# Optimization experiments

Hardware: AMD Instinct MI355X
Metric: run time of the kernel (lower is better)

## Reference

```python
import jax, jax.numpy as jnp
import numpy as np
import functools

N, D, R, E, L, C, MAXDEG = 40000, 128, 3, 640000, 2, 40, 512
BN_EPS = 1e-5


def setup_inputs():
    ks = iter(jax.random.split(jax.random.key(0), 40))
    nrm = lambda s, sc=0.05: jax.random.normal(next(ks), s, dtype=jnp.float32) * sc
    x = jax.random.normal(next(ks), (N, D), dtype=jnp.float32)
    edge_indices = jax.random.randint(next(ks), (R, 2, E), 0, N, dtype=jnp.int32)
    out_emb = nrm((L, MAXDEG, D)).at[:, 0].set(0.0)  # padding_idx=0 -> zero row
    in_emb = nrm((L, MAXDEG, D)).at[:, 0].set(0.0)
    return dict(
        x=x, edge_indices=edge_indices,
        W_src=nrm((L, D, D)), b_src=nrm((L, D)),
        W_dst=nrm((L, D, D)), b_dst=nrm((L, D)),
        W_outf=nrm((L, D)), b_outf=nrm((L,)),
        W_inf=nrm((L, D)), b_inf=nrm((L,)),
        W_fc=nrm((L, D, D)), b_fc=nrm((L, D)),
        bn_gamma=jnp.ones((L, D), jnp.float32), bn_beta=jnp.zeros((L, D), jnp.float32),
        out_deg_emb=out_emb, in_deg_emb=in_emb,
        out_mask=jnp.ones((R, N), jnp.float32), out_mask_bias=jnp.zeros((R, N), jnp.float32),
        in_mask=jnp.ones((R, N), jnp.float32), in_mask_bias=jnp.zeros((R, N), jnp.float32),
        alpha=jnp.float32(0.5), tau=jnp.float32(0.0),
        W_lin=nrm((D, C)), b_lin=nrm((C,)),
    )


def _forward(x, W_src, b_src, W_dst, b_dst, W_outf, b_outf, W_inf, b_inf,
             W_fc, b_fc, bn_gamma, bn_beta, out_deg_emb, in_deg_emb,
             out_mask, out_mask_bias, in_mask, in_mask_bias, alpha, tau,
             W_lin, b_lin, edge_indices):
    seg = lambda d, i: jax.ops.segment_sum(d, i, num_segments=N)
    # source builds I with arange(0, N-1): identity with last diagonal entry missing
    i_mask = (jnp.arange(N) < N - 1).astype(jnp.float32)[:, None]

    rel = []
    for r in range(R):
        row, col = edge_indices[r, 0], edge_indices[r, 1]
        ones = jnp.ones(E, jnp.float32)
        out_deg, in_deg = seg(ones, row), seg(ones, col)
        ods = jnp.where(out_deg > 0, 1.0 / jnp.sqrt(jnp.maximum(out_deg, 1.0)), 0.0)
        ids_ = jnp.where(in_deg > 0, 1.0 / jnp.sqrt(jnp.maximum(in_deg, 1.0)), 0.0)
        # 'dir' norm: D_out^{-1/2} A D_in^{-1/2}; the transposed adj shares the same edge weights
        w = ods[row] * ids_[col]
        rel.append((row, col, w,
                    jnp.clip(out_deg, 0, MAXDEG - 1).astype(jnp.int32),
                    jnp.clip(in_deg, 0, MAXDEG - 1).astype(jnp.int32)))

    def spmm(r_, y):  # adj_norm @ y : gather cols, scatter-add to rows
        row, col, w = rel[r_][0], rel[r_][1], rel[r_][2]
        return seg(w[:, None] * y[col], row)

    def spmm_t(r_, y):  # adj_norm^T @ y
        row, col, w = rel[r_][0], rel[r_][1], rel[r_][2]
        return seg(w[:, None] * y[row], col)

    def dirichlet(mm, y):
        x1 = y / (jnp.sum(jnp.abs(y), axis=1, keepdims=True) + 1e-12)  # row_l1_normalize
        x1sq = x1 * x1
        return (i_mask * x1sq + mm(x1sq)) - 2.0 * ((i_mask * x1 + mm(x1)) * x1 - x1sq)

    eff_tau = jnp.exp(tau) + 0.1

    def conv(l, h):
        out = jnp.zeros((N, D), h.dtype)
        cis, cos_ = [], []
        for r in range(R):
            mm = functools.partial(spmm, r)
            mmt = functools.partial(spmm_t, r)
            out_nei, in_nei = mm(h), mmt(h)
            e_out, e_in = dirichlet(mm, h), dirichlet(mmt, h)
            c_out = (-e_out + out_deg_emb[l][rel[r][3]]) @ W_outf[l] + b_outf[l]  # [N]
            c_in = (-e_in + in_deg_emb[l][rel[r][4]]) @ W_inf[l] + b_inf[l]
            cm = jax.nn.softmax(jnp.stack([c_out, c_in], axis=1) / eff_tau, axis=1)  # tau_softmax
            c_out = cm[:, 0] * out_mask[r] + out_mask_bias[r]
            c_in = cm[:, 1] * in_mask[r] + in_mask_bias[r]
            out = out + c_out[:, None] * (out_nei @ W_src[l] + b_src[l]) \
                      + c_in[:, None] * (in_nei @ W_dst[l] + b_dst[l])
            cis.append(c_in)
            cos_.append(c_out)
        out = out / R
        # F.pad(x,(0,dim-x.shape[1])) is a no-op since input_dim == output_dim
        output = out + alpha * (h @ W_fc[l] + b_fc[l])
        mu, var = jnp.mean(output, axis=0), jnp.var(output, axis=0)  # BatchNorm1d (train mode)
        output = (output - mu) / jnp.sqrt(var + BN_EPS) * bn_gamma[l] + bn_beta[l]
        return output, jnp.mean(jnp.stack(cis), 0)[:, None], jnp.mean(jnp.stack(cos_), 0)[:, None]

    pos_h, neg_h = x, x
    pos_hs, neg_hs, gs, cins, couts = [], [], [], [], []
    for l in range(L):
        ph, ci, co = conv(l, pos_h)
        ph = jax.nn.relu(ph)  # jumping_knowledge truthy -> relu every layer; dropout p=0
        perm = jax.random.permutation(jax.random.key(100 + l), N)  # torch.randperm
        nh, _, _ = conv(l, neg_h[perm])
        nh = jax.nn.relu(nh)
        pos_h, neg_h = ph, nh
        pos_hs.append(ph)
        neg_hs.append(nh)
        gs.append(jnp.mean(ph, axis=0, keepdims=True))
        cins.append(ci)
        couts.append(co)
    c_ins = jnp.mean(jnp.stack(cins), 0)
    c_outs = jnp.mean(jnp.stack(couts), 0)
    jk = functools.reduce(jnp.maximum, pos_hs)  # JumpingKnowledge mode='max'
    logp = jax.nn.log_softmax(jk @ W_lin + b_lin, axis=1)
    return (logp, c_ins, c_outs, *pos_hs, *neg_hs, *gs)


def reference(x, edge_indices, W_src, b_src, W_dst, b_dst, W_outf, b_outf,
              W_inf, b_inf, W_fc, b_fc, bn_gamma, bn_beta, out_deg_emb,
              in_deg_emb, out_mask, out_mask_bias, in_mask, in_mask_bias,
              alpha, tau, W_lin, b_lin):
    return _forward(x, W_src, b_src, W_dst, b_dst, W_outf, b_outf, W_inf, b_inf,
                    W_fc, b_fc, bn_gamma, bn_beta, out_deg_emb, in_deg_emb,
                    out_mask, out_mask_bias, in_mask, in_mask_bias, alpha, tau,
                    W_lin, b_lin, edge_indices)
```

## Files before the change

### kernel.cpp

```cpp
#include <hip/hip_runtime.h>

constexpr int Nn = 40000;
constexpr int Dd = 128;
constexpr int Rr = 3;
constexpr int Ee = 640000;
constexpr int Ll = 2;
constexpr int Cc = 40;
constexpr int MAXD = 512;
constexpr float BN_EPS = 1e-5f;

constexpr int RB_ELEMS = 1024;
constexpr int RB_NB = (Nn + RB_ELEMS - 1) / RB_ELEMS;
constexpr int RB_BINS = 256;
constexpr int RB_H = RB_BINS * RB_NB;

constexpr int EB_ELEMS = 4096;
constexpr int EB_NB = (Ee + EB_ELEMS - 1) / EB_ELEMS;
constexpr int EB_H = 256 * EB_NB;

constexpr int HR_BINS = 13334;
constexpr int HR_PAD = 13344;
constexpr int HR_SB = 16;
constexpr int HR_CHUNK = (Ee + HR_SB - 1) / HR_SB;

__device__ __forceinline__ unsigned rotl32(unsigned x, int d) { return (x << d) | (x >> (32 - d)); }

__device__ void threefry2x32(unsigned k0, unsigned k1, unsigned c0, unsigned c1,
                             unsigned& o0, unsigned& o1) {
  unsigned ks2 = k0 ^ k1 ^ 0x1BD11BDAu;
  unsigned x0 = c0 + k0, x1 = c1 + k1;
#define TFR4(a,b,c,d2) \
  x0 += x1; x1 = rotl32(x1,a);  x1 ^= x0; \
  x0 += x1; x1 = rotl32(x1,b);  x1 ^= x0; \
  x0 += x1; x1 = rotl32(x1,c);  x1 ^= x0; \
  x0 += x1; x1 = rotl32(x1,d2); x1 ^= x0;
  TFR4(13,15,26,6);  x0 += k1;  x1 += ks2 + 1u;
  TFR4(17,29,16,24); x0 += ks2; x1 += k0 + 2u;
  TFR4(13,15,26,6);  x0 += k0;  x1 += k1 + 3u;
  TFR4(17,29,16,24); x0 += k1;  x1 += ks2 + 4u;
  TFR4(13,15,26,6);  x0 += ks2; x1 += k0 + 5u;
#undef TFR4
  o0 = x0; o1 = x1;
}

__global__ void k_genkeys2(unsigned* __restrict__ keys, unsigned seed0, unsigned seed1,
                           int rounds, int* __restrict__ vout, int doIota) {
  int i = blockIdx.x * blockDim.x + threadIdx.x;
  if (i >= 2 * Nn) return;
  int seg = i / Nn, li = i - seg * Nn;
  unsigned seed = seg ? seed1 : seed0;
  unsigned k0 = 0u, k1 = seed, sk0 = 0u, sk1 = 0u;
  for (int rd = 0; rd < rounds; rd++) {
    unsigned a0, a1, b0, b1;
    threefry2x32(k0, k1, 0u, 0u, a0, a1);
    threefry2x32(k0, k1, 0u, 1u, b0, b1);
    sk0 = b0; sk1 = b1;
    k0 = a0; k1 = a1;
  }
  unsigned o0, o1;
  threefry2x32(sk0, sk1, 0u, (unsigned)li, o0, o1);
  keys[i] = o0 ^ o1;
  if (doIota) vout[i] = li;
}

__global__ void k_rhist2(const unsigned* __restrict__ keys, int* __restrict__ hist, int shift) {
  __shared__ int lh[RB_BINS];
  int a = blockIdx.x / RB_NB, blk = blockIdx.x % RB_NB;
  const unsigned* src = keys + (size_t)a * Nn;
  int t = threadIdx.x;
  lh[t] = 0;
  __syncthreads();
  int base = blk * RB_ELEMS;
  for (int i = t; i < RB_ELEMS; i += 256) {
    int g = base + i;
    if (g < Nn) atomicAdd(&lh[(src[g] >> shift) & 255], 1);
  }
  __syncthreads();
  hist[(size_t)a * RB_H + t * RB_NB + blk] = lh[t];
}

__device__ void scan_body(const int* cnt, int* off, int n, int items) {
  int t = threadIdx.x;
  int lo = t * items, hi = min(lo + items, n);
  int s = 0;
  for (int i = lo; i < hi; i++) s += cnt[i];
  int lane = t & 63, wid = t >> 6;
  int sc = s;
#pragma unroll
  for (int o = 1; o < 64; o <<= 1) {
    int v = __shfl_up(sc, o);
    if (lane >= o) sc += v;
  }
  __shared__ int wsum[16], woff[16];
  if (lane == 63) wsum[wid] = sc;
  __syncthreads();
  if (t == 0) {
    int a = 0;
    for (int w = 0; w < 16; w++) { woff[w] = a; a += wsum[w]; }
    off[n] = a;
  }
  __syncthreads();
  int run = woff[wid] + sc - s;
  for (int i = lo; i < hi; i++) {
    int v = cnt[i];
    off[i] = run;
    run += v;
  }
}

__global__ __launch_bounds__(1024) void k_scanP(const int* __restrict__ hist, int* __restrict__ esc) {
  int a = blockIdx.x;
  scan_body(hist + (size_t)a * RB_H, esc + (size_t)a * (RB_H + 1), RB_H, (RB_H + 1023) / 1024);
}

__global__ __launch_bounds__(1024) void k_scan6(const int* __restrict__ odeg, const int* __restrict__ ideg,
                                                int* __restrict__ csr_off, int* __restrict__ csc_off) {
  int b = blockIdx.x;
  const int* cnt = (b < 3) ? (odeg + b * Nn) : (ideg + (b - 3) * Nn);
  int* off = (b < 3) ? (csr_off + b * (Nn + 1)) : (csc_off + (b - 3) * (Nn + 1));
  scan_body(cnt, off, Nn, (Nn + 1023) / 1024);
}

__global__ void k_rscatter2(const unsigned* __restrict__ keys, const int* __restrict__ vals,
                            const int* __restrict__ scanned, int shift,
                            unsigned* __restrict__ okeys, int* __restrict__ ovals) {
  __shared__ int running[RB_BINS];
  __shared__ int wcount[4][RB_BINS];
  __shared__ int dbase[RB_BINS];
  int a = blockIdx.x / RB_NB, blk = blockIdx.x % RB_NB;
  const unsigned* ksrc = keys + (size_t)a * Nn;
  const int* vsrc = vals + (size_t)a * Nn;
  unsigned* kdst = okeys + (size_t)a * Nn;
  int* vdst = ovals + (size_t)a * Nn;
  int t = threadIdx.x;
  int lane = t & 63, w = t >> 6;
  running[t] = 0;
  dbase[t] = scanned[(size_t)a * (RB_H + 1) + t * RB_NB + blk];
  int base = blk * RB_ELEMS;
  for (int rnd = 0; rnd < 4; rnd++) {
#pragma unroll
    for (int q = 0; q < 4; q++) wcount[q][t] = 0;
    __syncthreads();
    int g = base + rnd * 256 + t;
    bool valid = g < Nn;
    unsigned key = valid ? ksrc[g] : 0u;
    int d = (key >> shift) & 255;
    unsigned long long bb = __ballot(valid);
    unsigned long long mask = bb;
#pragma unroll
    for (int k = 0; k < 8; k++) {
      bool b = (d >> k) & 1;
      unsigned long long tt = __ballot(b && valid);
      mask &= b ? tt : ~tt;
    }
    mask &= bb;
    int riw = __popcll(mask & ((1ull << lane) - 1ull));
    int cnt_ = __popcll(mask);
    if (valid && riw == 0) wcount[w][d] = cnt_;
    __syncthreads();
    if (valid) {
      int prior = 0;
#pragma unroll
      for (int ww = 0; ww < 4; ww++) if (ww < w) prior += wcount[ww][d];
      int gp = dbase[d] + running[d] + prior + riw;
      kdst[gp] = key;
      vdst[gp] = vsrc[g];
    }
    __syncthreads();
    running[t] += wcount[0][t] + wcount[1][t] + wcount[2][t] + wcount[3][t];
    __syncthreads();
  }
}

__global__ void k_permrows(const float* __restrict__ src, const int* __restrict__ perm,
                           float* __restrict__ dst) {
  int row = blockIdx.x * 8 + (threadIdx.x >> 5);
  int lane = threadIdx.x & 31;
  if (row >= Nn) return;
  int p = perm[row];
  ((float4*)(dst + (size_t)row * Dd))[lane] = ((const float4*)(src + (size_t)p * Dd))[lane];
}

__global__ __launch_bounds__(256) void k_hist2(const int* __restrict__ ei, int* __restrict__ partials) {
  __shared__ int lh[HR_BINS];
  int bid = blockIdx.x;
  int sb = bid % HR_SB;
  int range = (bid / HR_SB) % 3;
  int j = bid / (3 * HR_SB);
  int rel = j >> 1, which = j & 1;
  const int* src = ei + (size_t)rel * 2 * Ee + (size_t)which * Ee;
  int lo = range * HR_BINS;
  for (int i = threadIdx.x; i < HR_BINS; i += 256) lh[i] = 0;
  __syncthreads();
  int e0 = sb * HR_CHUNK, e1 = min(e0 + HR_CHUNK, Ee);
  for (int e = e0 + threadIdx.x; e < e1; e += 256) {
    int v = src[e] - lo;
    if (v >= 0 && v < HR_BINS) atomicAdd(&lh[v], 1);
  }
  __syncthreads();
  int* dst = partials + (size_t)bid * HR_PAD;
  for (int i = threadIdx.x; i < HR_BINS; i += 256) dst[i] = lh[i];
}

__global__ void k_hreduce(const int* __restrict__ partials, int* __restrict__ odeg,
                          int* __restrict__ ideg) {
  int idx = blockIdx.x * 256 + threadIdx.x;
  if (idx >= 6 * Nn) return;
  int j = idx / Nn, bin = idx - j * Nn;
  int range = bin / HR_BINS, off = bin - range * HR_BINS;
  const int* p = partials + (size_t)((j * 3 + range) * HR_SB) * HR_PAD + off;
  int sum = 0;
#pragma unroll
  for (int b = 0; b < HR_SB; b++) sum += p[(size_t)b * HR_PAD];
  int rel = j >> 1;
  (j & 1 ? ideg : odeg)[rel * Nn + bin] = sum;
}

__global__ void k_degnorm(const int* __restrict__ odeg, const int* __restrict__ ideg,
                          float* __restrict__ ods, float* __restrict__ ids,
                          int* __restrict__ odix, int* __restrict__ idix) {
  int idx = blockIdx.x * blockDim.x + threadIdx.x;
  if (idx >= Rr * Nn) return;
  int od = odeg[idx], id_ = ideg[idx];
  ods[idx] = od > 0 ? 1.0f / sqrtf((float)od) : 0.0f;
  ids[idx] = id_ > 0 ? 1.0f / sqrtf((float)id_) : 0.0f;
  odix[idx] = od < MAXD - 1 ? od : MAXD - 1;
  idix[idx] = id_ < MAXD - 1 ? id_ : MAXD - 1;
}

__global__ void k_pack(const int* __restrict__ ei, unsigned* __restrict__ pcsr,
                       unsigned* __restrict__ pcsc) {
  int idx = blockIdx.x * 256 + threadIdx.x;
  if (idx >= 3 * Ee) return;
  int r = idx / Ee, e = idx - r * Ee;
  const int* base = ei + (size_t)r * 2 * Ee;
  unsigned rw = (unsigned)base[e], cl = (unsigned)base[Ee + e];
  pcsr[idx] = (rw << 16) | cl;
  pcsc[idx] = (cl << 16) | rw;
}

__global__ __launch_bounds__(256) void k_ehist(const unsigned* __restrict__ pin,
                                               int* __restrict__ hist, int shift) {
  __shared__ int lh[256];
  int a = blockIdx.x / EB_NB, blk = blockIdx.x % EB_NB;
  const unsigned* src = pin + (size_t)a * Ee;
  lh[threadIdx.x] = 0;
  __syncthreads();
  int base = blk * EB_ELEMS;
  for (int i = threadIdx.x; i < EB_ELEMS; i += 256) {
    int g = base + i;
    if (g < Ee) atomicAdd(&lh[(src[g] >> shift) & 255], 1);
  }
  __syncthreads();
  hist[(size_t)a * EB_H + threadIdx.x * EB_NB + blk] = lh[threadIdx.x];
}

__global__ __launch_bounds__(1024) void k_escan6(const int* __restrict__ hist, int* __restrict__ esc) {
  int a = blockIdx.x;
  scan_body(hist + (size_t)a * EB_H, esc + (size_t)a * (EB_H + 1), EB_H, (EB_H + 1023) / 1024);
}

__global__ __launch_bounds__(256) void k_escatter(const unsigned* __restrict__ pin,
                                                  const int* __restrict__ esc, int shift,
                                                  unsigned* __restrict__ pout) {
  __shared__ int running[256];
  __shared__ int wcount[4][256];
  __shared__ int dbase[256];
  int a = blockIdx.x / EB_NB, blk = blockIdx.x % EB_NB;
  const unsigned* src = pin + (size_t)a * Ee;
  unsigned* dst = pout + (size_t)a * Ee;
  int t = threadIdx.x;
  int lane = t & 63, w = t >> 6;
  running[t] = 0;
  dbase[t] = esc[(size_t)a * (EB_H + 1) + t * EB_NB + blk];
  int base = blk * EB_ELEMS;
  for (int rnd = 0; rnd < 16; rnd++) {
#pragma unroll
    for (int q = 0; q < 4; q++) wcount[q][t] = 0;
    __syncthreads();
    int g = base + rnd * 256 + t;
    bool valid = g < Ee;
    unsigned key = valid ? src[g] : 0u;
    int d = (key >> shift) & 255;
    unsigned long long bb = __ballot(valid);
    unsigned long long mask = bb;
#pragma unroll
    for (int k = 0; k < 8; k++) {
      bool b = (d >> k) & 1;
      unsigned long long tt = __ballot(b && valid);
      mask &= b ? tt : ~tt;
    }
    mask &= bb;
    int riw = __popcll(mask & ((1ull << lane) - 1ull));
    int cnt_ = __popcll(mask);
    if (valid && riw == 0) wcount[w][d] = cnt_;
    __syncthreads();
    if (valid) {
      int prior = 0;
#pragma unroll
      for (int ww = 0; ww < 4; ww++) if (ww < w) prior += wcount[ww][d];
      int gp = dbase[d] + running[d] + prior + riw;
      dst[gp] = key;
    }
    __syncthreads();
    running[t] += wcount[0][t] + wcount[1][t] + wcount[2][t] + wcount[3][t];
    __syncthreads();
  }
}

__global__ void k_rowscalar(const float* __restrict__ h, const float* __restrict__ Wfo,
                            const float* __restrict__ Wfi, float4* __restrict__ aux,
                            const float* __restrict__ ods, const float* __restrict__ ids,
                            float4* __restrict__ auxrd,
                            float* __restrict__ bnsum, float* __restrict__ gs) {
  if (blockIdx.x == 0) {
    bnsum[threadIdx.x] = 0.f;
    if (gs != nullptr && threadIdx.x < Dd) gs[threadIdx.x] = 0.f;
  }
  int wid = (blockIdx.x * blockDim.x + threadIdx.x) >> 6;
  int lane = threadIdx.x & 63;
  if (wid >= Nn) return;
  float2 a = ((const float2*)(h + (size_t)wid * Dd))[lane];
  float2 wo = ((const float2*)Wfo)[lane];
  float2 wi = ((const float2*)Wfi)[lane];
  float l1 = fabsf(a.x) + fabsf(a.y);
  float so = a.x * a.x * wo.x + a.y * a.y * wo.y;
  float si = a.x * a.x * wi.x + a.y * a.y * wi.y;
#pragma unroll
  for (int o = 32; o; o >>= 1) {
    l1 += __shfl_xor(l1, o);
    so += __shfl_xor(so, o);
    si += __shfl_xor(si, o);
  }
  if (lane == 0) {
    float ri = 1.0f / (l1 + 1e-12f);
    float qo = ri * ri * so, qi = ri * ri * si;
    aux[wid] = make_float4(ri, qo, qi, 0.f);
#pragma unroll
    for (int r = 0; r < Rr; r++) {
      auxrd[(size_t)(2 * r) * Nn + wid] = make_float4(ids[r * Nn + wid], ri, qo, 0.f);
      auxrd[(size_t)(2 * r + 1) * Nn + wid] = make_float4(ods[r * Nn + wid], ri, qi, 0.f);
    }
  }
}

__global__ void k_lut2(const float* __restrict__ eo, const float* __restrict__ ei_,
                       const float* __restrict__ W_outf, const float* __restrict__ W_inf,
                       float* __restrict__ luto, float* __restrict__ luti) {
  int wid = (blockIdx.x * blockDim.x + threadIdx.x) >> 6;
  int lane = threadIdx.x & 63;
  if (wid >= 2 * MAXD) return;
  int l = wid >> 9, k = wid & (MAXD - 1);
  float2 a = ((const float2*)(eo + ((size_t)l * MAXD + k) * Dd))[lane];
  float2 b = ((const float2*)(ei_ + ((size_t)l * MAXD + k) * Dd))[lane];
  float2 wo = ((const float2*)(W_outf + l * Dd))[lane];
  float2 wi = ((const float2*)(W_inf + l * Dd))[lane];
  float so = a.x * wo.x + a.y * wo.y;
  float si = b.x * wi.x + b.y * wi.y;
#pragma unroll
  for (int o = 32; o; o >>= 1) { so += __shfl_xor(so, o); si += __shfl_xor(si, o); }
  if (lane == 0) { luto[wid] = so; luti[wid] = si; }
}

__global__ __launch_bounds__(256) void k_csrdir3(
    const int* __restrict__ csr_off, const unsigned* __restrict__ pcsr,
    const int* __restrict__ csc_off, const unsigned* __restrict__ pcsc,
    const float* __restrict__ ods_r, const float* __restrict__ ids_r,
    const float4* __restrict__ auxo, const float4* __restrict__ auxi,
    const float4* __restrict__ aux, const float* __restrict__ h,
    const float* __restrict__ Wfo, const float* __restrict__ Wfi,
    const float* __restrict__ luto, const float* __restrict__ luti,
    const int* __restrict__ odix, const int* __restrict__ idix,
    const float* __restrict__ bo, const float* __restrict__ bi,
    const float* __restrict__ taup,
    const float* __restrict__ omask, const float* __restrict__ omaskb,
    const float* __restrict__ imask, const float* __restrict__ imaskb,
    float* __restrict__ Tout, float* __restrict__ Tin,
    float* __restrict__ sco, float* __restrict__ sci,
    float* __restrict__ co_acc, float* __restrict__ ci_acc,
    int first, int is_pos) {
  __shared__ float lq[4], lp[4], lc[4];
  int t = threadIdx.x;
  int wv = t >> 6, lane = t & 63;
  int dir = wv >> 1;
  int n = blockIdx.x * 2 + (wv & 1);
  const int* off = dir ? csc_off : csr_off;
  const unsigned* nbrp = dir ? pcsc : pcsr;
  const float4* auxd = dir ? auxi : auxo;
  float a_self = (dir ? ids_r : ods_r)[n];
  const float* Wf = dir ? Wfi : Wfo;
  int s0 = off[n], s1 = off[n + 1];
  int hl = lane & 31, half = lane >> 5;
  float4 wf4 = ((const float4*)Wf)[hl];
  float4 hn4 = ((const float4*)(h + (size_t)n * Dd))[hl];
  float rn = aux[n].x;
  float4 s = make_float4(0.f, 0.f, 0.f, 0.f);
  float4 pa = make_float4(0.f, 0.f, 0.f, 0.f);
  float qacc = 0.f;
  for (int base = s0; base < s1; base += 64) {
    int eidx = base + lane;
    bool valid = eidx < s1;
    int mi = valid ? (int)(nbrp[eidx] & 0xFFFFu) : 0;
    float4 av = valid ? auxd[mi] : make_float4(0.f, 0.f, 0.f, 0.f);
    int cnt = min(64, s1 - base);
#pragma unroll 4
    for (int j = half; j < cnt; j += 2) {
      int m = __shfl(mi, j);
      float sc = __shfl(av.x, j);
      float rm = __shfl(av.y, j);
      float qv = __shfl(av.z, j);
      float w = a_self * sc;
      float wrm = w * rm;
      float4 hv = ((const float4*)(h + (size_t)m * Dd))[hl];
      s.x += w * hv.x; s.y += w * hv.y; s.z += w * hv.z; s.w += w * hv.w;
      pa.x += wrm * hv.x; pa.y += wrm * hv.y; pa.z += wrm * hv.z; pa.w += wrm * hv.w;
      qacc += w * qv;
    }
  }
  s.x += __shfl_xor(s.x, 32); s.y += __shfl_xor(s.y, 32);
  s.z += __shfl_xor(s.z, 32); s.w += __shfl_xor(s.w, 32);
  pa.x += __shfl_xor(pa.x, 32); pa.y += __shfl_xor(pa.y, 32);
  pa.z += __shfl_xor(pa.z, 32); pa.w += __shfl_xor(pa.w, 32);
  qacc += __shfl_xor(qacc, 32);
  float pd = rn * (hn4.x * wf4.x * pa.x + hn4.y * wf4.y * pa.y +
                   hn4.z * wf4.z * pa.z + hn4.w * wf4.w * pa.w);
#pragma unroll
  for (int o = 16; o; o >>= 1) pd += __shfl_xor(pd, o);
  if (lane == 0) { lq[wv] = qacc; lp[wv] = pd; }
  __syncthreads();
  if (t < 2) {
    int nn = blockIdx.x * 2 + t;
    float Qo_ = lq[t], Po_ = lp[t], Qi_ = lq[2 + t], Pi_ = lp[2 + t];
    float4 a2 = aux[nn];
    float im = (nn < Nn - 1) ? 1.0f : 0.0f;
    float so_ = luto[odix[nn]] + bo[0] - (Qo_ - 2.0f * Po_ + (2.0f - im) * a2.y);
    float si_ = luti[idix[nn]] + bi[0] - (Qi_ - 2.0f * Pi_ + (2.0f - im) * a2.z);
    float tt = expf(taup[0]) + 0.1f;
    float aa = so_ / tt, bb = si_ / tt;
    float mm = fmaxf(aa, bb);
    float ea = expf(aa - mm), eb = expf(bb - mm);
    float inv = 1.0f / (ea + eb);
    float co = ea * inv * omask[nn] + omaskb[nn];
    float ci = eb * inv * imask[nn] + imaskb[nn];
    lc[t] = co; lc[2 + t] = ci;
    if (first) { sco[nn] = co; sci[nn] = ci; }
    else       { sco[nn] += co; sci[nn] += ci; }
    if (is_pos) { co_acc[nn] += co; ci_acc[nn] += ci; }
  }
  __syncthreads();
  float c = lc[wv];
  if (lane < 32) {
    float* T = dir ? Tin : Tout;
    size_t o = (size_t)n * Dd;
    float4 v = make_float4(c * s.x, c * s.y, c * s.z, c * s.w);
    if (!first) {
      float4 old = ((const float4*)(T + o))[hl];
      v.x += old.x; v.y += old.y; v.z += old.z; v.w += old.w;
    }
    ((float4*)(T + o))[hl] = v;
  }
}

__global__ __launch_bounds__(256) void k_gemmconv(
    const float* __restrict__ Tout, const float* __restrict__ Tin, const float* __restrict__ h,
    const float* __restrict__ Wsrc, const float* __restrict__ Wdst, const float* __restrict__ Wfc,
    const float* __restrict__ bsrc, const float* __restrict__ bdst, const float* __restrict__ bfc,
    const float* __restrict__ sco, const float* __restrict__ sci,
    const float* __restrict__ alphap, float* __restrict__ pre, float* __restrict__ bnsum) {
  __shared__ float Asm[64][36];
  __shared__ float Bsm[32][132];
  __shared__ float lsum[128], lsum2[128];
  int t = threadIdx.x;
  int rg = t >> 5, cg = t & 31;
  int m0 = blockIdx.x * 64;
  int arow = t >> 2, aq = t & 3;
  float alpha = alphap[0];
  float acc[8][4];
#pragma unroll
  for (int r = 0; r < 8; r++)
#pragma unroll
    for (int c = 0; c < 4; c++) acc[r][c] = 0.f;
  for (int kt = 0; kt < 12; kt++) {
    int sec = kt >> 2, kc = (kt & 3) * 32;
    const float* Ap = sec == 0 ? Tout : (sec == 1 ? Tin : h);
    const float* Wp = sec == 0 ? Wsrc : (sec == 1 ? Wdst : Wfc);
    float sA = (sec == 2) ? alpha : (1.0f / (float)Rr);
    __syncthreads();
    {
      const float4* src = (const float4*)(Ap + (size_t)(m0 + arow) * Dd + kc + aq * 8);
      float4 v0 = src[0], v1 = src[1];
      float4* d0 = (float4*)&Asm[arow][aq * 8];
      d0[0] = make_float4(v0.x * sA, v0.y * sA, v0.z * sA, v0.w * sA);
      d0[1] = make_float4(v1.x * sA, v1.y * sA, v1.z * sA, v1.w * sA);
    }
#pragma unroll
    for (int j = 0; j < 4; j++) {
      int idx = t + j * 256;
      int k = idx >> 5, d4 = idx & 31;
      *(float4*)&Bsm[k][d4 * 4] = *(const float4*)(Wp + (size_t)(kc + k) * Dd + d4 * 4);
    }
    __syncthreads();
#pragma unroll
    for (int kk = 0; kk < 32; kk += 4) {
      float4 af[8], bf[4];
#pragma unroll
      for (int r = 0; r < 8; r++) af[r] = *(const float4*)&Asm[rg * 8 + r][kk];
#pragma unroll
      for (int j = 0; j < 4; j++) bf[j] = *(const float4*)&Bsm[kk + j][cg * 4];
#pragma unroll
      for (int r = 0; r < 8; r++) {
        const float* ap = (const float*)&af[r];
#pragma unroll
        for (int j = 0; j < 4; j++) {
          const float* bp = (const float*)&bf[j];
          acc[r][0] += ap[j] * bp[0];
          acc[r][1] += ap[j] * bp[1];
          acc[r][2] += ap[j] * bp[2];
          acc[r][3] += ap[j] * bp[3];
        }
      }
    }
  }
  float4 vb1 = *(const float4*)(bsrc + cg * 4);
  float4 vb2 = *(const float4*)(bdst + cg * 4);
  float4 vbf = *(const float4*)(bfc + cg * 4);
  float ps[4] = {0.f, 0.f, 0.f, 0.f}, ps2[4] = {0.f, 0.f, 0.f, 0.f};
#pragma unroll
  for (int r = 0; r < 8; r++) {
    int row = m0 + rg * 8 + r;
    size_t o = (size_t)row * Dd + cg * 4;
    float s1 = sco[row] * (1.0f / (float)Rr), s2 = sci[row] * (1.0f / (float)Rr);
    float4 v;
    v.x = acc[r][0] + s1 * vb1.x + s2 * vb2.x + alpha * vbf.x;
    v.y = acc[r][1] + s1 * vb1.y + s2 * vb2.y + alpha * vbf.y;
    v.z = acc[r][2] + s1 * vb1.z + s2 * vb2.z + alpha * vbf.z;
    v.w = acc[r][3] + s1 * vb1.w + s2 * vb2.w + alpha * vbf.w;
    *(float4*)(pre + o) = v;
    ps[0] += v.x; ps[1] += v.y; ps[2] += v.z; ps[3] += v.w;
    ps2[0] += v.x * v.x; ps2[1] += v.y * v.y; ps2[2] += v.z * v.z; ps2[3] += v.w * v.w;
  }
  if (t < 128) { lsum[t] = 0.f; lsum2[t] = 0.f; }
  __syncthreads();
#pragma unroll
  for (int j = 0; j < 4; j++) {
    atomicAdd(&lsum[cg * 4 + j], ps[j]);
    atomicAdd(&lsum2[cg * 4 + j], ps2[j]);
  }
  __syncthreads();
  if (t < 128) atomicAdd(&bnsum[t], lsum[t]);
  else if (t < 256) atomicAdd(&bnsum[t], lsum2[t - 128]);
}

__global__ void k_bnapply(const float* __restrict__ pre, const float* __restrict__ sums,
                          const float* __restrict__ gamma, const float* __restrict__ beta,
                          float* __restrict__ hout, float* __restrict__ gs, int do_gs) {
  __shared__ float ls[256];
  int c = threadIdx.x & 127, sub = threadIdx.x >> 7;
  float mu = sums[c] * (1.0f / (float)Nn);
  float var = sums[c + 128] * (1.0f / (float)Nn) - mu * mu;
  float sc = gamma[c] / sqrtf(var + BN_EPS);
  float bt = beta[c];
  float g = 0.f;
  for (int n = blockIdx.x * 2 + sub; n < Nn; n += gridDim.x * 2) {
    float v = (pre[(size_t)n * Dd + c] - mu) * sc + bt;
    v = fmaxf(v, 0.f);
    hout[(size_t)n * Dd + c] = v;
    g += v;
  }
  if (do_gs) {
    ls[threadIdx.x] = g;
    __syncthreads();
    if (sub == 0) atomicAdd(&gs[c], (ls[c] + ls[c + 128]) * (1.0f / (float)Nn));
  }
}

__global__ __launch_bounds__(64) void k_logp(const float* __restrict__ ph0, const float* __restrict__ ph1,
                      const float* __restrict__ Wlin, const float* __restrict__ blin,
                      const float* __restrict__ ci_acc, const float* __restrict__ co_acc,
                      float* __restrict__ cins, float* __restrict__ couts,
                      float* __restrict__ logp) {
  __shared__ float jk[Dd];
  __shared__ float lg[Cc];
  int n = blockIdx.x, t = threadIdx.x;
  if (t == 63) {
    cins[n] = ci_acc[n] * (1.0f / (float)(Ll * Rr));
    couts[n] = co_acc[n] * (1.0f / (float)(Ll * Rr));
  }
  for (int d = t; d < Dd; d += 64) jk[d] = fmaxf(ph0[(size_t)n * Dd + d], ph1[(size_t)n * Dd + d]);
  __syncthreads();
  if (t < Cc) {
    float acc = blin[t];
    for (int k = 0; k < Dd; k++) acc += jk[k] * Wlin[k * Cc + t];
    lg[t] = acc;
  }
  __syncthreads();
  float m = -1e30f;
  for (int c = 0; c < Cc; c++) m = fmaxf(m, lg[c]);
  float s = 0.f;
  for (int c = 0; c < Cc; c++) s += expf(lg[c] - m);
  float lse = m + logf(s);
  if (t < Cc) logp[(size_t)n * Cc + t] = lg[t] - lse;
}

extern "C" void kernel_launch(void* const* d_in, const int* in_sizes, int n_in,
                              void* d_out, int out_size, void* d_ws, size_t ws_size,
                              hipStream_t stream) {
  const float* x      = (const float*)d_in[0];
  const int*   ei     = (const int*)d_in[1];
  const float* W_src  = (const float*)d_in[2];
  const float* b_src  = (const float*)d_in[3];
  const float* W_dst  = (const float*)d_in[4];
  const float* b_dst  = (const float*)d_in[5];
  const float* W_outf = (const float*)d_in[6];
  const float* b_outf = (const float*)d_in[7];
  const float* W_inf  = (const float*)d_in[8];
  const float* b_inf  = (const float*)d_in[9];
  const float* W_fc   = (const float*)d_in[10];
  const float* b_fc   = (const float*)d_in[11];
  const float* gamma  = (const float*)d_in[12];
  const float* beta   = (const float*)d_in[13];
  const float* oemb   = (const float*)d_in[14];
  const float* iemb   = (const float*)d_in[15];
  const float* omask  = (const float*)d_in[16];
  const float* omaskb = (const float*)d_in[17];
  const float* imask  = (const float*)d_in[18];
  const float* imaskb = (const float*)d_in[19];
  const float* alphap = (const float*)d_in[20];
  const float* taup   = (const float*)d_in[21];
  const float* Wlin   = (const float*)d_in[22];
  const float* blin   = (const float*)d_in[23];

  float* out   = (float*)d_out;
  float* logp  = out;
  float* cins  = logp + (size_t)Nn * Cc;
  float* couts = cins + Nn;
  float* ph0   = couts + Nn;
  float* ph1   = ph0 + (size_t)Nn * Dd;
  float* nh0   = ph1 + (size_t)Nn * Dd;
  float* nh1   = nh0 + (size_t)Nn * Dd;
  float* gs0   = nh1 + (size_t)Nn * Dd;
  float* gs1   = gs0 + Dd;

  char* p = (char*)d_ws;
  auto alloc = [&](size_t bytes) -> void* {
    void* q = (void*)p;
    p += (bytes + 255) & ~(size_t)255;
    return q;
  };
  float* pre   = (float*)alloc((size_t)Nn * Dd * 4);
  float* Tout  = (float*)alloc((size_t)Nn * Dd * 4);
  float* Tin   = (float*)alloc((size_t)Nn * Dd * 4);
  float* hperm = (float*)alloc((size_t)Nn * Dd * 4);
  unsigned* pbuf = (unsigned*)alloc((size_t)6 * Ee * 4);
  size_t qwords = (size_t)6 * Ee;
  size_t pwords = (size_t)(6 * 3 * HR_SB) * HR_PAD;
  unsigned* qbuf = (unsigned*)alloc((qwords > pwords ? qwords : pwords) * 4);
  int* partials = (int*)qbuf;
  int* csr_off = (int*)alloc((size_t)Rr * (Nn + 1) * 4);
  int* csc_off = (int*)alloc((size_t)Rr * (Nn + 1) * 4);
  int* odeg    = (int*)alloc((size_t)Rr * Nn * 4);
  int* ideg    = (int*)alloc((size_t)Rr * Nn * 4);
  float* ods   = (float*)alloc((size_t)Rr * Nn * 4);
  float* ids   = (float*)alloc((size_t)Rr * Nn * 4);
  int* odix    = (int*)alloc((size_t)Rr * Nn * 4);
  int* idix    = (int*)alloc((size_t)Rr * Nn * 4);
  float4* aux  = (float4*)alloc((size_t)Nn * 16);
  float4* auxrd = (float4*)alloc((size_t)6 * Nn * 16);
  float* sco   = (float*)alloc((size_t)Nn * 4 * 2);
  float* sci   = sco + Nn;
  float* coacc = (float*)alloc((size_t)Nn * 4 * 2);
  float* ciacc = coacc + Nn;
  float* luto  = (float*)alloc((size_t)2 * MAXD * 4);
  float* luti  = (float*)alloc((size_t)2 * MAXD * 4);
  float* bnsum = (float*)alloc(256 * 4);
  unsigned* kbuf0 = (unsigned*)alloc((size_t)2 * Nn * 4);
  unsigned* kbuf1 = (unsigned*)alloc((size_t)2 * Nn * 4);
  int* vbuf0 = (int*)alloc((size_t)2 * Nn * 4);
  int* vbuf1 = (int*)alloc((size_t)2 * Nn * 4);
  int* rhist = (int*)alloc((size_t)2 * (RB_H + 1) * 4);
  int* rscan = (int*)alloc((size_t)2 * (RB_H + 1) * 4);
  int* ehist = (int*)alloc((size_t)6 * EB_H * 4);
  int* escan = (int*)alloc((size_t)6 * (EB_H + 1) * 4);

  k_hist2<<<6 * 3 * HR_SB, 256, 0, stream>>>(ei, partials);
  k_hreduce<<<(6 * Nn + 255) / 256, 256, 0, stream>>>(partials, odeg, ideg);
  k_degnorm<<<(Rr * Nn + 255) / 256, 256, 0, stream>>>(odeg, ideg, ods, ids, odix, idix);
  k_scan6<<<6, 1024, 0, stream>>>(odeg, ideg, csr_off, csc_off);
  k_pack<<<(3 * Ee + 255) / 256, 256, 0, stream>>>(ei, pbuf, pbuf + (size_t)3 * Ee);
  k_ehist<<<6 * EB_NB, 256, 0, stream>>>(pbuf, ehist, 16);
  k_escan6<<<6, 1024, 0, stream>>>(ehist, escan);
  k_escatter<<<6 * EB_NB, 256, 0, stream>>>(pbuf, escan, 16, qbuf);
  k_ehist<<<6 * EB_NB, 256, 0, stream>>>(qbuf, ehist, 24);
  k_escan6<<<6, 1024, 0, stream>>>(ehist, escan);
  k_escatter<<<6 * EB_NB, 256, 0, stream>>>(qbuf, escan, 24, pbuf);
  hipMemsetAsync(coacc, 0, (size_t)Nn * 4 * 2, stream);
  k_lut2<<<2 * MAXD / 4, 256, 0, stream>>>(oemb, iemb, W_outf, W_inf, luto, luti);

  auto radix4b = [&]() {
    for (int pass = 0; pass < 4; pass++) {
      const unsigned* ik = (pass & 1) ? kbuf1 : kbuf0;
      const int*      iv = (pass & 1) ? vbuf1 : vbuf0;
      unsigned*       ok = (pass & 1) ? kbuf0 : kbuf1;
      int*            ov = (pass & 1) ? vbuf0 : vbuf1;
      int shift = pass * 8;
      k_rhist2<<<2 * RB_NB, 256, 0, stream>>>(ik, rhist, shift);
      k_scanP<<<2, 1024, 0, stream>>>(rhist, rscan);
      k_rscatter2<<<2 * RB_NB, 256, 0, stream>>>(ik, iv, rscan, shift, ok, ov);
    }
  };
  k_genkeys2<<<(2 * Nn + 255) / 256, 256, 0, stream>>>(kbuf0, 100u, 101u, 1, vbuf0, 1);
  radix4b();
  k_genkeys2<<<(2 * Nn + 255) / 256, 256, 0, stream>>>(kbuf0, 100u, 101u, 2, vbuf0, 0);
  radix4b();

  auto conv = [&](int l, const float* hin, float* hout, float* gs, int is_pos) {
    const float* Wfo = W_outf + l * Dd;
    const float* Wfi = W_inf + l * Dd;
    k_rowscalar<<<Nn / 4, 256, 0, stream>>>(hin, Wfo, Wfi, aux, ods, ids, auxrd, bnsum,
                                            is_pos ? gs : nullptr);
    for (int r = 0; r < Rr; r++) {
      k_csrdir3<<<Nn / 2, 256, 0, stream>>>(csr_off + r * (Nn + 1), pbuf + (size_t)r * Ee,
                                            csc_off + r * (Nn + 1), pbuf + (size_t)(3 + r) * Ee,
                                            ods + r * Nn, ids + r * Nn,
                                            auxrd + (size_t)(2 * r) * Nn,
                                            auxrd + (size_t)(2 * r + 1) * Nn,
                                            aux, hin, Wfo, Wfi,
                                            luto + l * MAXD, luti + l * MAXD,
                                            odix + r * Nn, idix + r * Nn,
                                            b_outf + l, b_inf + l, taup,
                                            omask + (size_t)r * Nn, omaskb + (size_t)r * Nn,
                                            imask + (size_t)r * Nn, imaskb + (size_t)r * Nn,
                                            Tout, Tin, sco, sci, coacc, ciacc,
                                            r == 0 ? 1 : 0, is_pos);
    }
    k_gemmconv<<<Nn / 64, 256, 0, stream>>>(Tout, Tin, hin,
                                            W_src + (size_t)l * Dd * Dd, W_dst + (size_t)l * Dd * Dd,
                                            W_fc + (size_t)l * Dd * Dd,
                                            b_src + l * Dd, b_dst + l * Dd, b_fc + l * Dd,
                                            sco, sci, alphap, pre, bnsum);
    k_bnapply<<<256, 256, 0, stream>>>(pre, bnsum, gamma + l * Dd, beta + l * Dd, hout, gs, is_pos);
  };

  conv(0, x, ph0, gs0, 1);
  k_permrows<<<Nn / 8, 256, 0, stream>>>(x, vbuf0, hperm);
  conv(0, hperm, nh0, nullptr, 0);

  conv(1, ph0, ph1, gs1, 1);
  k_permrows<<<Nn / 8, 256, 0, stream>>>(nh0, vbuf0 + Nn, hperm);
  conv(1, hperm, nh1, nullptr, 0);

  k_logp<<<Nn, 64, 0, stream>>>(ph0, ph1, Wlin, blin, ciacc, coacc, cins, couts, logp);
}
```

Baseline: 2.277 ms.

## Batch positive and negative conv passes into single doubled-grid launches

The positive and negative (row-permuted) graph convolutions for each layer now run together. Every kernel launches with a doubled grid and picks its input by block index, with per-matrix aux, T, sco/sci, pre and bnsum buffers. This halves the number of launches and gives each launch more blocks to fill the GPU, and the CSR neighbour structure is shared and may stay cache-resident across both matrices. In exchange it needs twice the intermediate buffer memory, and the larger per-launch working set could reduce cache hit rates.

```diff
diff --git a/kernel.cpp b/kernel.cpp
--- a/kernel.cpp
+++ b/kernel.cpp
@@ -308,16 +308,22 @@
   }
 }
 
-__global__ void k_rowscalar(const float* __restrict__ h, const float* __restrict__ Wfo,
-                            const float* __restrict__ Wfi, float4* __restrict__ aux,
+__global__ void k_rowscalar(const float* __restrict__ hA, const float* __restrict__ hB,
+                            const float* __restrict__ Wfo, const float* __restrict__ Wfi,
+                            float4* __restrict__ aux,
                             const float* __restrict__ ods, const float* __restrict__ ids,
                             float4* __restrict__ auxrd,
                             float* __restrict__ bnsum, float* __restrict__ gs) {
   if (blockIdx.x == 0) {
     bnsum[threadIdx.x] = 0.f;
+    bnsum[256 + threadIdx.x] = 0.f;
     if (gs != nullptr && threadIdx.x < Dd) gs[threadIdx.x] = 0.f;
   }
-  int wid = (blockIdx.x * blockDim.x + threadIdx.x) >> 6;
+  int half = Nn / 4;
+  int mat = blockIdx.x >= half ? 1 : 0;
+  int lb = blockIdx.x - mat * half;
+  const float* h = mat ? hB : hA;
+  int wid = (lb * blockDim.x + threadIdx.x) >> 6;
   int lane = threadIdx.x & 63;
   if (wid >= Nn) return;
   float2 a = ((const float2*)(h + (size_t)wid * Dd))[lane];
@@ -335,11 +341,12 @@
   if (lane == 0) {
     float ri = 1.0f / (l1 + 1e-12f);
     float qo = ri * ri * so, qi = ri * ri * si;
-    aux[wid] = make_float4(ri, qo, qi, 0.f);
+    aux[(size_t)mat * Nn + wid] = make_float4(ri, qo, qi, 0.f);
+    float4* ard = auxrd + (size_t)mat * 6 * Nn;
 #pragma unroll
     for (int r = 0; r < Rr; r++) {
-      auxrd[(size_t)(2 * r) * Nn + wid] = make_float4(ids[r * Nn + wid], ri, qo, 0.f);
-      auxrd[(size_t)(2 * r + 1) * Nn + wid] = make_float4(ods[r * Nn + wid], ri, qi, 0.f);
+      ard[(size_t)(2 * r) * Nn + wid] = make_float4(ids[r * Nn + wid], ri, qo, 0.f);
+      ard[(size_t)(2 * r + 1) * Nn + wid] = make_float4(ods[r * Nn + wid], ri, qi, 0.f);
     }
   }
 }
@@ -366,8 +373,9 @@
     const int* __restrict__ csr_off, const unsigned* __restrict__ pcsr,
     const int* __restrict__ csc_off, const unsigned* __restrict__ pcsc,
     const float* __restrict__ ods_r, const float* __restrict__ ids_r,
-    const float4* __restrict__ auxo, const float4* __restrict__ auxi,
-    const float4* __restrict__ aux, const float* __restrict__ h,
+    const float4* __restrict__ auxrd_base, int rel,
+    const float4* __restrict__ aux_base,
+    const float* __restrict__ hA, const float* __restrict__ hB,
     const float* __restrict__ Wfo, const float* __restrict__ Wfi,
     const float* __restrict__ luto, const float* __restrict__ luti,
     const int* __restrict__ odix, const int* __restrict__ idix,
@@ -375,18 +383,25 @@
     const float* __restrict__ taup,
     const float* __restrict__ omask, const float* __restrict__ omaskb,
     const float* __restrict__ imask, const float* __restrict__ imaskb,
-    float* __restrict__ Tout, float* __restrict__ Tin,
-    float* __restrict__ sco, float* __restrict__ sci,
+    float* __restrict__ Tout_base, float* __restrict__ Tin_base,
+    float* __restrict__ sco_base, float* __restrict__ sci_base,
     float* __restrict__ co_acc, float* __restrict__ ci_acc,
-    int first, int is_pos) {
+    int first) {
   __shared__ float lq[4], lp[4], lc[4];
+  int halfg = Nn / 2;
+  int mat = blockIdx.x >= halfg ? 1 : 0;
+  int blk = blockIdx.x - mat * halfg;
+  const float* h = mat ? hB : hA;
+  const float4* aux = aux_base + (size_t)mat * Nn;
+  float* sco = sco_base + (size_t)mat * Nn;
+  float* sci = sci_base + (size_t)mat * Nn;
   int t = threadIdx.x;
   int wv = t >> 6, lane = t & 63;
   int dir = wv >> 1;
-  int n = blockIdx.x * 2 + (wv & 1);
+  int n = blk * 2 + (wv & 1);
   const int* off = dir ? csc_off : csr_off;
   const unsigned* nbrp = dir ? pcsc : pcsr;
-  const float4* auxd = dir ? auxi : auxo;
+  const float4* auxd = auxrd_base + (size_t)mat * 6 * Nn + (size_t)(2 * rel + dir) * Nn;
   float a_self = (dir ? ids_r : ods_r)[n];
   const float* Wf = dir ? Wfi : Wfo;
   int s0 = off[n], s1 = off[n + 1];
@@ -429,7 +444,7 @@
   if (lane == 0) { lq[wv] = qacc; lp[wv] = pd; }
   __syncthreads();
   if (t < 2) {
-    int nn = blockIdx.x * 2 + t;
+    int nn = blk * 2 + t;
     float Qo_ = lq[t], Po_ = lp[t], Qi_ = lq[2 + t], Pi_ = lp[2 + t];
     float4 a2 = aux[nn];
     float im = (nn < Nn - 1) ? 1.0f : 0.0f;
@@ -445,12 +460,12 @@
     lc[t] = co; lc[2 + t] = ci;
     if (first) { sco[nn] = co; sci[nn] = ci; }
     else       { sco[nn] += co; sci[nn] += ci; }
-    if (is_pos) { co_acc[nn] += co; ci_acc[nn] += ci; }
+    if (mat == 0) { co_acc[nn] += co; ci_acc[nn] += ci; }
   }
   __syncthreads();
   float c = lc[wv];
   if (lane < 32) {
-    float* T = dir ? Tin : Tout;
+    float* T = (dir ? Tin_base : Tout_base) + (size_t)mat * Nn * Dd;
     size_t o = (size_t)n * Dd;
     float4 v = make_float4(c * s.x, c * s.y, c * s.z, c * s.w);
     if (!first) {
@@ -462,17 +477,28 @@
 }
 
 __global__ __launch_bounds__(256) void k_gemmconv(
-    const float* __restrict__ Tout, const float* __restrict__ Tin, const float* __restrict__ h,
+    const float* __restrict__ Tout_base, const float* __restrict__ Tin_base,
+    const float* __restrict__ hA, const float* __restrict__ hB,
     const float* __restrict__ Wsrc, const float* __restrict__ Wdst, const float* __restrict__ Wfc,
     const float* __restrict__ bsrc, const float* __restrict__ bdst, const float* __restrict__ bfc,
-    const float* __restrict__ sco, const float* __restrict__ sci,
-    const float* __restrict__ alphap, float* __restrict__ pre, float* __restrict__ bnsum) {
+    const float* __restrict__ sco_base, const float* __restrict__ sci_base,
+    const float* __restrict__ alphap, float* __restrict__ pre_base, float* __restrict__ bnsum_base) {
   __shared__ float Asm[64][36];
   __shared__ float Bsm[32][132];
   __shared__ float lsum[128], lsum2[128];
+  int halfg = Nn / 64;
+  int mat = blockIdx.x >= halfg ? 1 : 0;
+  int mb = blockIdx.x - mat * halfg;
+  const float* Tout = Tout_base + (size_t)mat * Nn * Dd;
+  const float* Tin = Tin_base + (size_t)mat * Nn * Dd;
+  const float* h = mat ? hB : hA;
+  const float* sco = sco_base + (size_t)mat * Nn;
+  const float* sci = sci_base + (size_t)mat * Nn;
+  float* pre = pre_base + (size_t)mat * Nn * Dd;
+  float* bnsum = bnsum_base + (size_t)mat * 256;
   int t = threadIdx.x;
   int rg = t >> 5, cg = t & 31;
-  int m0 = blockIdx.x * 64;
+  int m0 = mb * 64;
   int arow = t >> 2, aq = t & 3;
   float alpha = alphap[0];
   float acc[8][4];
@@ -551,23 +577,29 @@
   else if (t < 256) atomicAdd(&bnsum[t], lsum2[t - 128]);
 }
 
-__global__ void k_bnapply(const float* __restrict__ pre, const float* __restrict__ sums,
+__global__ void k_bnapply(const float* __restrict__ pre_base, const float* __restrict__ bnsum_base,
                           const float* __restrict__ gamma, const float* __restrict__ beta,
-                          float* __restrict__ hout, float* __restrict__ gs, int do_gs) {
+                          float* __restrict__ houtA, float* __restrict__ houtB,
+                          float* __restrict__ gs) {
   __shared__ float ls[256];
+  int mat = blockIdx.x >= 256 ? 1 : 0;
+  int blk = blockIdx.x - mat * 256;
+  const float* pre = pre_base + (size_t)mat * Nn * Dd;
+  const float* sums = bnsum_base + (size_t)mat * 256;
+  float* hout = mat ? houtB : houtA;
   int c = threadIdx.x & 127, sub = threadIdx.x >> 7;
   float mu = sums[c] * (1.0f / (float)Nn);
   float var = sums[c + 128] * (1.0f / (float)Nn) - mu * mu;
   float sc = gamma[c] / sqrtf(var + BN_EPS);
   float bt = beta[c];
   float g = 0.f;
-  for (int n = blockIdx.x * 2 + sub; n < Nn; n += gridDim.x * 2) {
+  for (int n = blk * 2 + sub; n < Nn; n += 512) {
     float v = (pre[(size_t)n * Dd + c] - mu) * sc + bt;
     v = fmaxf(v, 0.f);
     hout[(size_t)n * Dd + c] = v;
     g += v;
   }
-  if (do_gs) {
+  if (mat == 0) {
     ls[threadIdx.x] = g;
     __syncthreads();
     if (sub == 0) atomicAdd(&gs[c], (ls[c] + ls[c + 128]) * (1.0f / (float)Nn));
@@ -647,9 +679,9 @@
     p += (bytes + 255) & ~(size_t)255;
     return q;
   };
-  float* pre   = (float*)alloc((size_t)Nn * Dd * 4);
-  float* Tout  = (float*)alloc((size_t)Nn * Dd * 4);
-  float* Tin   = (float*)alloc((size_t)Nn * Dd * 4);
+  float* pre2  = (float*)alloc((size_t)2 * Nn * Dd * 4);
+  float* Tout2 = (float*)alloc((size_t)2 * Nn * Dd * 4);
+  float* Tin2  = (float*)alloc((size_t)2 * Nn * Dd * 4);
   float* hperm = (float*)alloc((size_t)Nn * Dd * 4);
   unsigned* pbuf = (unsigned*)alloc((size_t)6 * Ee * 4);
   size_t qwords = (size_t)6 * Ee;
@@ -664,15 +696,15 @@
   float* ids   = (float*)alloc((size_t)Rr * Nn * 4);
   int* odix    = (int*)alloc((size_t)Rr * Nn * 4);
   int* idix    = (int*)alloc((size_t)Rr * Nn * 4);
-  float4* aux  = (float4*)alloc((size_t)Nn * 16);
-  float4* auxrd = (float4*)alloc((size_t)6 * Nn * 16);
-  float* sco   = (float*)alloc((size_t)Nn * 4 * 2);
-  float* sci   = sco + Nn;
+  float4* aux2 = (float4*)alloc((size_t)2 * Nn * 16);
+  float4* auxrd2 = (float4*)alloc((size_t)2 * 6 * Nn * 16);
+  float* sco2  = (float*)alloc((size_t)2 * Nn * 4);
+  float* sci2  = (float*)alloc((size_t)2 * Nn * 4);
   float* coacc = (float*)alloc((size_t)Nn * 4 * 2);
   float* ciacc = coacc + Nn;
   float* luto  = (float*)alloc((size_t)2 * MAXD * 4);
   float* luti  = (float*)alloc((size_t)2 * MAXD * 4);
-  float* bnsum = (float*)alloc(256 * 4);
+  float* bnsum2 = (float*)alloc(512 * 4);
   unsigned* kbuf0 = (unsigned*)alloc((size_t)2 * Nn * 4);
   unsigned* kbuf1 = (unsigned*)alloc((size_t)2 * Nn * 4);
   int* vbuf0 = (int*)alloc((size_t)2 * Nn * 4);
@@ -713,41 +745,40 @@
   k_genkeys2<<<(2 * Nn + 255) / 256, 256, 0, stream>>>(kbuf0, 100u, 101u, 2, vbuf0, 0);
   radix4b();
 
-  auto conv = [&](int l, const float* hin, float* hout, float* gs, int is_pos) {
+  auto biconv = [&](int l, const float* hA, const float* hB,
+                    float* houtA, float* houtB, float* gs) {
     const float* Wfo = W_outf + l * Dd;
     const float* Wfi = W_inf + l * Dd;
-    k_rowscalar<<<Nn / 4, 256, 0, stream>>>(hin, Wfo, Wfi, aux, ods, ids, auxrd, bnsum,
-                                            is_pos ? gs : nullptr);
+    k_rowscalar<<<2 * (Nn / 4), 256, 0, stream>>>(hA, hB, Wfo, Wfi, aux2, ods, ids, auxrd2,
+                                                  bnsum2, gs);
     for (int r = 0; r < Rr; r++) {
-      k_csrdir3<<<Nn / 2, 256, 0, stream>>>(csr_off + r * (Nn + 1), pbuf + (size_t)r * Ee,
-                                            csc_off + r * (Nn + 1), pbuf + (size_t)(3 + r) * Ee,
-                                            ods + r * Nn, ids + r * Nn,
-                                            auxrd + (size_t)(2 * r) * Nn,
-                                            auxrd + (size_t)(2 * r + 1) * Nn,
-                                            aux, hin, Wfo, Wfi,
-                                            luto + l * MAXD, luti + l * MAXD,
-                                            odix + r * Nn, idix + r * Nn,
-                                            b_outf + l, b_inf + l, taup,
-                                            omask + (size_t)r * Nn, omaskb + (size_t)r * Nn,
-                                            imask + (size_t)r * Nn, imaskb + (size_t)r * Nn,
-                                            Tout, Tin, sco, sci, coacc, ciacc,
-                                            r == 0 ? 1 : 0, is_pos);
-    }
-    k_gemmconv<<<Nn / 64, 256, 0, stream>>>(Tout, Tin, hin,
-                                            W_src + (size_t)l * Dd * Dd, W_dst + (size_t)l * Dd * Dd,
-                                            W_fc + (size_t)l * Dd * Dd,
-                                            b_src + l * Dd, b_dst + l * Dd, b_fc + l * Dd,
-                                            sco, sci, alphap, pre, bnsum);
-    k_bnapply<<<256, 256, 0, stream>>>(pre, bnsum, gamma + l * Dd, beta + l * Dd, hout, gs, is_pos);
+      k_csrdir3<<<2 * (Nn / 2), 256, 0, stream>>>(csr_off + r * (Nn + 1), pbuf + (size_t)r * Ee,
+                                                  csc_off + r * (Nn + 1), pbuf + (size_t)(3 + r) * Ee,
+                                                  ods + r * Nn, ids + r * Nn,
+                                                  auxrd2, r, aux2, hA, hB, Wfo, Wfi,
+                                                  luto + l * MAXD, luti + l * MAXD,
+                                                  odix + r * Nn, idix + r * Nn,
+                                                  b_outf + l, b_inf + l, taup,
+                                                  omask + (size_t)r * Nn, omaskb + (size_t)r * Nn,
+                                                  imask + (size_t)r * Nn, imaskb + (size_t)r * Nn,
+                                                  Tout2, Tin2, sco2, sci2, coacc, ciacc,
+                                                  r == 0 ? 1 : 0);
+    }
+    k_gemmconv<<<2 * (Nn / 64), 256, 0, stream>>>(Tout2, Tin2, hA, hB,
+                                                  W_src + (size_t)l * Dd * Dd,
+                                                  W_dst + (size_t)l * Dd * Dd,
+                                                  W_fc + (size_t)l * Dd * Dd,
+                                                  b_src + l * Dd, b_dst + l * Dd, b_fc + l * Dd,
+                                                  sco2, sci2, alphap, pre2, bnsum2);
+    k_bnapply<<<512, 256, 0, stream>>>(pre2, bnsum2, gamma + l * Dd, beta + l * Dd,
+                                       houtA, houtB, gs);
   };
 
-  conv(0, x, ph0, gs0, 1);
   k_permrows<<<Nn / 8, 256, 0, stream>>>(x, vbuf0, hperm);
-  conv(0, hperm, nh0, nullptr, 0);
-
-  conv(1, ph0, ph1, gs1, 1);
+  biconv(0, x, hperm, ph0, nh0, gs0);
+
   k_permrows<<<Nn / 8, 256, 0, stream>>>(nh0, vbuf0 + Nn, hperm);
-  conv(1, hperm, nh1, nullptr, 0);
+  biconv(1, ph0, hperm, ph1, nh1, gs1);
 
   k_logp<<<Nn, 64, 0, stream>>>(ph0, ph1, Wlin, blin, ciacc, coacc, cins, couts, logp);
 }
```

New measurement: 2.162 ms. 5.0% less time.
